# Kernel optimization log

Hardware: AMD Instinct MI355X
Metric: run time of the kernel (lower is better)

Reference implementation:

```python
import jax, jax.numpy as jnp
import numpy as np

N, E, D, H, ED, L = 50000, 800000, 256, 8, 16, 6
C = D // H  # 32
NEG_SLOPE = 0.2
EPS = 1e-5


def setup_inputs() -> dict:
    key = jax.random.key(0)
    ks = jax.random.split(key, 16)
    f32 = jnp.float32
    return {
        "x": jax.random.normal(ks[0], (N, D), f32),
        "edge_index": jax.random.randint(ks[1], (2, E), 0, N, dtype=jnp.int64),
        "edge_attr": jax.random.normal(ks[2], (E, ED), f32),
        # shared GATConv params (single conv reused every step, as in the source)
        "W": jax.random.normal(ks[3], (D, D), f32) / np.sqrt(D),
        "att_src": jax.random.normal(ks[4], (H, C), f32) * 0.05,
        "att_dst": jax.random.normal(ks[5], (H, C), f32) * 0.05,
        "att_edge": jax.random.normal(ks[6], (H, C), f32) * 0.05,
        "W_edge": jax.random.normal(ks[7], (ED, D), f32) / np.sqrt(ED),
        "bias": jnp.zeros((D,), f32),
        # per-step FFN + LayerNorm params
        "ffn_w1": jax.random.normal(ks[8], (L, D, 4 * D), f32) / np.sqrt(D),
        "ffn_b1": jnp.zeros((L, 4 * D), f32),
        "ffn_w2": jax.random.normal(ks[9], (L, 4 * D, D), f32) / np.sqrt(4 * D),
        "ffn_b2": jnp.zeros((L, D), f32),
        "ln1_g": jnp.ones((L, D), f32),
        "ln1_b": jnp.zeros((L, D), f32),
        "ln2_g": jnp.ones((L, D), f32),
        "ln2_b": jnp.zeros((L, D), f32),
    }


def _layernorm(x, g, b):
    mu = jnp.mean(x, -1, keepdims=True)
    var = jnp.mean(jnp.square(x - mu), -1, keepdims=True)
    return (x - mu) * jax.lax.rsqrt(var + EPS) * g + b


def _gat_conv(m, edge_index, edge_attr, W, att_src, att_dst, att_edge, W_edge, bias):
    n = m.shape[0]
    x_proj = (m @ W).reshape(n, H, C)  # [N,H,C]
    # add self loops; edge_attr fill_value='mean' (PyG default): mean of incoming edge feats
    src0, dst0 = edge_index[0], edge_index[1]
    deg = jax.ops.segment_sum(jnp.ones_like(dst0, jnp.float32), dst0, n)
    ea_mean = jax.ops.segment_sum(edge_attr, dst0, n) / jnp.maximum(deg, 1.0)[:, None]
    loop = jnp.arange(n, dtype=src0.dtype)
    src = jnp.concatenate([src0, loop])
    dst = jnp.concatenate([dst0, loop])
    ea = jnp.concatenate([edge_attr, ea_mean], 0)
    e_proj = (ea @ W_edge).reshape(-1, H, C)  # [E+N,H,C]
    a_src = jnp.sum(x_proj * att_src, -1)  # [N,H]
    a_dst = jnp.sum(x_proj * att_dst, -1)  # [N,H]
    a_edge = jnp.sum(e_proj * att_edge, -1)  # [E+N,H]
    alpha = jax.nn.leaky_relu(a_src[src] + a_dst[dst] + a_edge, NEG_SLOPE)
    # softmax over edges grouped by destination node
    amax = jax.ops.segment_max(alpha, dst, n)  # every node has a self loop
    ex = jnp.exp(alpha - amax[dst])
    denom = jax.ops.segment_sum(ex, dst, n)
    attn = ex / denom[dst]  # [E+N,H]
    msg = x_proj[src] * attn[:, :, None]  # [E+N,H,C]
    out = jax.ops.segment_sum(msg, dst, n).reshape(n, H * C)
    return out + bias


def reference(x, edge_index, edge_attr, W, att_src, att_dst, att_edge, W_edge, bias,
              ffn_w1, ffn_b1, ffn_w2, ffn_b2, ln1_g, ln1_b, ln2_g, ln2_b):
    m = x
    for i in range(L):
        g = _gat_conv(m, edge_index, edge_attr, W, att_src, att_dst, att_edge, W_edge, bias)
        m = _layernorm(g + m, ln1_g[i], ln1_b[i])  # dropout is identity in eval
        h = jax.nn.relu(m @ ffn_w1[i] + ffn_b1[i]) @ ffn_w2[i] + ffn_b2[i]
        m = _layernorm(h + m, ln2_g[i], ln2_b[i])
    return m
```

## Files before the change

### kernel.cpp

```cpp
#include <hip/hip_runtime.h>
#include <math.h>

#define NN 50000
#define MP 50048
#define EE 800000
#define DD 256
#define HH 8
#define CC 32
#define EDIMK 16
#define LL 6
#define HID 1024
#define NEG 0.2f
#define LNEPS 1e-5f
#define NPARTS ((NN + 255) / 256)

using short8   = __attribute__((ext_vector_type(8))) short;
using ushort8  = __attribute__((ext_vector_type(8))) unsigned short;
using floatx4  = __attribute__((ext_vector_type(4))) float;

static __device__ __forceinline__ float4 ld4(const float* p) {
    return *reinterpret_cast<const float4*>(p);
}
static __device__ __forceinline__ void st4(float* p, float4 v) {
    *reinterpret_cast<float4*>(p) = v;
}
static __device__ __forceinline__ float b2f(unsigned short u) {
    union { unsigned int i; float f; } v; v.i = ((unsigned int)u) << 16; return v.f;
}
static __device__ __forceinline__ unsigned short f2b(float f) {
    union { float f; unsigned int i; } v; v.f = f;
    unsigned int r = (v.i + 0x7fffu + ((v.i >> 16) & 1u)) >> 16;
    return (unsigned short)r;
}
static __device__ __forceinline__ void gload_lds16(const ushort* g, ushort* l) {
    __builtin_amdgcn_global_load_lds((const __attribute__((address_space(1))) void*)g,
                                     (__attribute__((address_space(3))) void*)l, 16, 0, 0);
}

__global__ void k_weh(const float* __restrict__ W_edge, const float* __restrict__ att_edge,
                      float* __restrict__ w_eh) {
    int t = threadIdx.x;
    if (t < EDIMK * HH) {
        int k = t >> 3, h = t & 7;
        float s = 0.f;
        for (int c = 0; c < CC; ++c) s += W_edge[k * DD + h * CC + c] * att_edge[h * CC + c];
        w_eh[t] = s;
    }
}

__global__ void k_edge_pre(const float* __restrict__ edge_attr, const int* __restrict__ ei,
                           const float* __restrict__ w_eh, float* __restrict__ a_edge,
                           int* __restrict__ deg) {
    __shared__ float sw[EDIMK * HH];
    if (threadIdx.x < EDIMK * HH) sw[threadIdx.x] = w_eh[threadIdx.x];
    __syncthreads();
    int e = blockIdx.x * blockDim.x + threadIdx.x;
    if (e >= EE) return;
    float ea[EDIMK];
#pragma unroll
    for (int k4 = 0; k4 < EDIMK; k4 += 4) {
        float4 v = ld4(edge_attr + (size_t)e * EDIMK + k4);
        ea[k4] = v.x; ea[k4 + 1] = v.y; ea[k4 + 2] = v.z; ea[k4 + 3] = v.w;
    }
#pragma unroll
    for (int h = 0; h < HH; ++h) {
        float s = 0.f;
#pragma unroll
        for (int k = 0; k < EDIMK; ++k) s += ea[k] * sw[k * HH + h];
        a_edge[(size_t)e * HH + h] = s;
    }
    atomicAdd(&deg[ei[EE + e]], 1);
}

__global__ __launch_bounds__(256) void k_scan1(const int* __restrict__ deg,
                                               int* __restrict__ rowptr,
                                               int* __restrict__ part) {
    __shared__ int wsum[4];
    int tid = threadIdx.x, wid = tid >> 6, lane = tid & 63;
    int g = blockIdx.x * 256 + tid;
    int v = (g < NN) ? deg[g] : 0;
    int s = v;
#pragma unroll
    for (int off = 1; off < 64; off <<= 1) {
        int t = __shfl_up(s, off, 64);
        if (lane >= off) s += t;
    }
    if (lane == 63) wsum[wid] = s;
    __syncthreads();
    int woff = 0;
    for (int i = 0; i < wid; ++i) woff += wsum[i];
    s += woff;
    if (g < NN) rowptr[g + 1] = s;
    if (tid == 255) part[blockIdx.x] = s;
}
__global__ __launch_bounds__(256) void k_scan2(int* __restrict__ part) {
    __shared__ int wsum[4];
    int tid = threadIdx.x, wid = tid >> 6, lane = tid & 63;
    int v = (tid < NPARTS) ? part[tid] : 0;
    int s = v;
#pragma unroll
    for (int off = 1; off < 64; off <<= 1) {
        int t = __shfl_up(s, off, 64);
        if (lane >= off) s += t;
    }
    if (lane == 63) wsum[wid] = s;
    __syncthreads();
    int woff = 0;
    for (int i = 0; i < wid; ++i) woff += wsum[i];
    s += woff;
    if (tid < NPARTS) part[tid] = s - v;
}
__global__ __launch_bounds__(256) void k_scan3(int* __restrict__ rowptr,
                                               const int* __restrict__ part) {
    int g = blockIdx.x * 256 + threadIdx.x;
    if (g == 0) rowptr[0] = 0;
    if (g < NN) rowptr[g + 1] += part[blockIdx.x];
}

__global__ void k_scatter(const int* __restrict__ ei, const int* __restrict__ rowptr,
                          int* __restrict__ cursor, int* __restrict__ s_src,
                          int* __restrict__ s_eid) {
    int e = blockIdx.x * blockDim.x + threadIdx.x;
    if (e >= EE) return;
    int dst = ei[EE + e];
    int p = rowptr[dst] + atomicAdd(&cursor[dst], 1);
    s_src[p] = ei[e];
    s_eid[p] = e;
}

__global__ void k_permute(const int* __restrict__ s_eid, const float* __restrict__ a_edge,
                          float* __restrict__ ae_csr) {
    size_t t = (size_t)blockIdx.x * blockDim.x + threadIdx.x;
    if (t >= (size_t)EE * HH) return;
    ae_csr[t] = a_edge[(size_t)s_eid[t >> 3] * HH + (t & 7)];
}

__global__ void k_selfmean(const int* __restrict__ rowptr, const float* __restrict__ ae_csr,
                           float* __restrict__ a_self) {
    int t = blockIdx.x * blockDim.x + threadIdx.x;
    if (t >= NN * HH) return;
    int n = t >> 3, h = t & 7;
    int k0 = rowptr[n], k1 = rowptr[n + 1];
    float s = 0.f;
    for (int k = k0; k < k1; ++k) s += ae_csr[(size_t)k * HH + h];
    int d = k1 - k0; if (d < 1) d = 1;
    a_self[t] = s / (float)d;
}

__global__ __launch_bounds__(1024) void k_trans(const float* __restrict__ src,
                                                ushort* __restrict__ dst, int K, int N) {
    __shared__ float s[32][33];
    const float* S = src + (size_t)blockIdx.z * K * N;
    ushort* D = dst + (size_t)blockIdx.z * K * N;
    int n0 = blockIdx.x * 32, k0 = blockIdx.y * 32;
    s[threadIdx.y][threadIdx.x] = S[(size_t)(k0 + threadIdx.y) * N + n0 + threadIdx.x];
    __syncthreads();
    D[(size_t)(n0 + threadIdx.y) * K + k0 + threadIdx.x] = f2b(s[threadIdx.x][threadIdx.y]);
}

__global__ void k_cvt(const float* __restrict__ x, float* __restrict__ m,
                      ushort* __restrict__ mb) {
    int t = blockIdx.x * blockDim.x + threadIdx.x;
    if (t >= NN * DD) return;
    float v = x[t];
    m[t] = v;
    mb[t] = f2b(v);
}

__global__ __launch_bounds__(256) void k_gemm_bf16(const ushort* __restrict__ A,
                                                   const ushort* __restrict__ Bt,
                                                   const float* __restrict__ bias,
                                                   void* __restrict__ Cout,
                                                   int Nc, int K, int mode) {
    __shared__ ushort As[128 * 64];
    __shared__ ushort Bs[128 * 64];
    int tid = threadIdx.x;
    int w = tid >> 6, lane = tid & 63;
    int tileM = blockIdx.y * 128, tileN = blockIdx.x * 128;
    const ushort* gA[4]; const ushort* gB[4];
    ushort* lA[4]; ushort* lB[4];
#pragma unroll
    for (int p = 0; p < 4; ++p) {
        int c = (p * 4 + w) * 64 + lane;
        int row = c >> 3, slot = c & 7;
        int gs = slot ^ (row & 7);
        gA[p] = A + (size_t)(tileM + row) * K + gs * 8;
        gB[p] = Bt + (size_t)(tileN + row) * K + gs * 8;
        lA[p] = As + (size_t)c * 8;
        lB[p] = Bs + (size_t)c * 8;
    }
    int wr = w >> 1, wc = w & 1;
    int fr = lane & 15, q = lane >> 4;
    floatx4 acc[4][4] = {};
    for (int k0 = 0; k0 < K; k0 += 64) {
        __syncthreads();
#pragma unroll
        for (int p = 0; p < 4; ++p) gload_lds16(gA[p] + k0, lA[p]);
#pragma unroll
        for (int p = 0; p < 4; ++p) gload_lds16(gB[p] + k0, lB[p]);
        __syncthreads();
#pragma unroll
        for (int kc = 0; kc < 2; ++kc) {
            int ps = ((kc * 4 + q) ^ (fr & 7)) * 8;
            short8 af[4], bf[4];
#pragma unroll
            for (int i = 0; i < 4; ++i)
                af[i] = *(const short8*)(As + (wr * 64 + i * 16 + fr) * 64 + ps);
#pragma unroll
            for (int j = 0; j < 4; ++j)
                bf[j] = *(const short8*)(Bs + (wc * 64 + j * 16 + fr) * 64 + ps);
#pragma unroll
            for (int i = 0; i < 4; ++i)
#pragma unroll
                for (int j = 0; j < 4; ++j)
                    acc[i][j] = __builtin_amdgcn_mfma_f32_16x16x32_bf16(af[i], bf[j], acc[i][j], 0, 0, 0);
        }
    }
    int rbase = tileM + wr * 64 + q * 4;
    int cbase = tileN + wc * 64 + fr;
#pragma unroll
    for (int j = 0; j < 4; ++j) {
        int col = cbase + j * 16;
        float bb = (mode != 1) ? bias[col] : 0.f;
#pragma unroll
        for (int i = 0; i < 4; ++i) {
            int row = rbase + i * 16;
#pragma unroll
            for (int r = 0; r < 4; ++r) {
                float v = acc[i][j][r] + bb;
                if (mode == 2 && v < 0.f) v = 0.f;
                ((ushort*)Cout)[(size_t)(row + r) * Nc + col] = f2b(v);
            }
        }
    }
}

__global__ __launch_bounds__(256) void k_gemm2_ln(const ushort* __restrict__ A,
                                                  const ushort* __restrict__ Bt,
                                                  const float* __restrict__ bias,
                                                  const float* __restrict__ gma,
                                                  const float* __restrict__ bta,
                                                  float* __restrict__ m,
                                                  ushort* __restrict__ mb,
                                                  int rowsValid) {
    __shared__ ushort As[64 * 64];
    __shared__ ushort Bs[256 * 64];
    __shared__ float redS[64][4];
    __shared__ float redQ[64][4];
    const int K = HID;
    int tid = threadIdx.x;
    int w = tid >> 6, lane = tid & 63;
    int tileM = blockIdx.x * 64;
    int rA = tid >> 3, sl = tid & 7;
    int gs = sl ^ (rA & 7);
    const ushort* gA = A + (size_t)(tileM + rA) * K + gs * 8;
    const ushort* gB = Bt + (size_t)rA * K + gs * 8;
    ushort* lA = As + (size_t)tid * 8;
    ushort* lB = Bs + (size_t)tid * 8;
    int fr = lane & 15, q = lane >> 4;
    floatx4 acc[4][4] = {};
    for (int k0 = 0; k0 < K; k0 += 64) {
        __syncthreads();
        gload_lds16(gA + k0, lA);
        gload_lds16(gA + (size_t)32 * K + k0, lA + 256 * 8);
#pragma unroll
        for (int p = 0; p < 8; ++p)
            gload_lds16(gB + (size_t)p * 32 * K + k0, lB + (size_t)p * 256 * 8);
        __syncthreads();
#pragma unroll
        for (int kc = 0; kc < 2; ++kc) {
            int ps = ((kc * 4 + q) ^ (fr & 7)) * 8;
            short8 af[4], bf[4];
#pragma unroll
            for (int i = 0; i < 4; ++i)
                af[i] = *(const short8*)(As + (i * 16 + fr) * 64 + ps);
#pragma unroll
            for (int j = 0; j < 4; ++j)
                bf[j] = *(const short8*)(Bs + (w * 64 + j * 16 + fr) * 64 + ps);
#pragma unroll
            for (int i = 0; i < 4; ++i)
#pragma unroll
                for (int j = 0; j < 4; ++j)
                    acc[i][j] = __builtin_amdgcn_mfma_f32_16x16x32_bf16(af[i], bf[j], acc[i][j], 0, 0, 0);
        }
    }
    int colb = w * 64 + fr;
    float bw[4], gw[4], btw[4];
#pragma unroll
    for (int j = 0; j < 4; ++j) {
        bw[j] = bias[colb + j * 16];
        gw[j] = gma[colb + j * 16];
        btw[j] = bta[colb + j * 16];
    }
#pragma unroll
    for (int i = 0; i < 4; ++i) {
#pragma unroll
        for (int rr = 0; rr < 4; ++rr) {
            int lrow = i * 16 + q * 4 + rr;
            int grow = tileM + lrow;
            bool valid = grow < rowsValid;
            float s = 0.f, s2 = 0.f;
#pragma unroll
            for (int j = 0; j < 4; ++j) {
                float rres = valid ? m[(size_t)grow * DD + colb + j * 16] : 0.f;
                float gv = acc[i][j][rr] + bw[j] + rres;
                acc[i][j][rr] = gv;
                s += gv; s2 += gv * gv;
            }
#pragma unroll
            for (int msk = 1; msk < 16; msk <<= 1) {
                s += __shfl_xor(s, msk, 16);
                s2 += __shfl_xor(s2, msk, 16);
            }
            if (fr == 0) { redS[lrow][w] = s; redQ[lrow][w] = s2; }
        }
    }
    __syncthreads();
#pragma unroll
    for (int i = 0; i < 4; ++i) {
#pragma unroll
        for (int rr = 0; rr < 4; ++rr) {
            int lrow = i * 16 + q * 4 + rr;
            int grow = tileM + lrow;
            if (grow >= rowsValid) continue;
            float su = redS[lrow][0] + redS[lrow][1] + redS[lrow][2] + redS[lrow][3];
            float sq = redQ[lrow][0] + redQ[lrow][1] + redQ[lrow][2] + redQ[lrow][3];
            float mu = su * (1.0f / DD);
            float var = sq * (1.0f / DD) - mu * mu;
            float rs = rsqrtf(var + LNEPS);
#pragma unroll
            for (int j = 0; j < 4; ++j) {
                float v = (acc[i][j][rr] - mu) * rs * gw[j] + btw[j];
                size_t idx = (size_t)grow * DD + colb + j * 16;
                m[idx] = v;
                mb[idx] = f2b(v);
            }
        }
    }
}

__global__ void k_srcdst(const ushort* __restrict__ xb, const float* __restrict__ att_src,
                         const float* __restrict__ att_dst, float* __restrict__ a_src,
                         float* __restrict__ a_dst) {
    __shared__ float ss[DD], sd[DD];
    int tid = threadIdx.x;
    if (tid < DD) { ss[tid] = att_src[tid]; sd[tid] = att_dst[tid]; }
    __syncthreads();
    int t = blockIdx.x * blockDim.x + tid;
    if (t >= NN * HH) return;
    int n = t >> 3, h = t & 7;
    const ushort* xp = xb + (size_t)n * DD + h * CC;
    float s1 = 0.f, s2 = 0.f;
#pragma unroll
    for (int c = 0; c < CC; c += 4) {
        ushort4 u = *(const ushort4*)(xp + c);
        float vx = b2f(u.x), vy = b2f(u.y), vz = b2f(u.z), vw = b2f(u.w);
        int b = h * CC + c;
        s1 += vx * ss[b] + vy * ss[b + 1] + vz * ss[b + 2] + vw * ss[b + 3];
        s2 += vx * sd[b] + vy * sd[b + 1] + vz * sd[b + 2] + vw * sd[b + 3];
    }
    a_src[t] = s1;
    a_dst[t] = s2;
}

__global__ __launch_bounds__(256) void k_agg(const ushort* __restrict__ xb,
                                             const float* __restrict__ a_src,
                                             const float* __restrict__ a_dst,
                                             const float* __restrict__ a_self,
                                             const int* __restrict__ rowptr,
                                             const int* __restrict__ s_src,
                                             const float* __restrict__ ae_csr,
                                             const float* __restrict__ bias,
                                             const float* __restrict__ gma,
                                             const float* __restrict__ bta,
                                             float* __restrict__ m,
                                             ushort* __restrict__ mb) {
    int wid = (blockIdx.x * blockDim.x + threadIdx.x) >> 6;
    int lane = threadIdx.x & 63;
    int n = wid * 2 + (lane >> 5);
    if (n >= NN) return;
    int hl = lane & 31, h = hl >> 2, c8 = hl * 8;
    float adn = a_dst[n * HH + h];
    float al0 = a_src[n * HH + h] + adn + a_self[n * HH + h];
    al0 = al0 > 0.f ? al0 : NEG * al0;
    float w0 = __expf(al0);
    ushort8 xs = *(const ushort8*)(xb + (size_t)n * DD + c8);
    float acc[8];
#pragma unroll
    for (int i = 0; i < 8; ++i) acc[i] = w0 * b2f(xs[i]);
    float den = w0;
    int k = rowptr[n], k1 = rowptr[n + 1];
    for (; k + 3 < k1; k += 4) {
        int s0 = s_src[k], s1 = s_src[k + 1], s2 = s_src[k + 2], s3 = s_src[k + 3];
        float e0 = ae_csr[(size_t)k * HH + h];
        float e1 = ae_csr[(size_t)(k + 1) * HH + h];
        float e2 = ae_csr[(size_t)(k + 2) * HH + h];
        float e3 = ae_csr[(size_t)(k + 3) * HH + h];
        float t0 = a_src[(size_t)s0 * HH + h] + adn + e0;
        float t1 = a_src[(size_t)s1 * HH + h] + adn + e1;
        float t2 = a_src[(size_t)s2 * HH + h] + adn + e2;
        float t3 = a_src[(size_t)s3 * HH + h] + adn + e3;
        ushort8 v0 = *(const ushort8*)(xb + (size_t)s0 * DD + c8);
        ushort8 v1 = *(const ushort8*)(xb + (size_t)s1 * DD + c8);
        ushort8 v2 = *(const ushort8*)(xb + (size_t)s2 * DD + c8);
        ushort8 v3 = *(const ushort8*)(xb + (size_t)s3 * DD + c8);
        t0 = t0 > 0.f ? t0 : NEG * t0;
        t1 = t1 > 0.f ? t1 : NEG * t1;
        t2 = t2 > 0.f ? t2 : NEG * t2;
        t3 = t3 > 0.f ? t3 : NEG * t3;
        float wv0 = __expf(t0), wv1 = __expf(t1), wv2 = __expf(t2), wv3 = __expf(t3);
        den += (wv0 + wv1) + (wv2 + wv3);
#pragma unroll
        for (int i = 0; i < 8; ++i)
            acc[i] += (wv0 * b2f(v0[i]) + wv1 * b2f(v1[i])) + (wv2 * b2f(v2[i]) + wv3 * b2f(v3[i]));
    }
    for (; k < k1; ++k) {
        int s0 = s_src[k];
        float t0 = a_src[(size_t)s0 * HH + h] + adn + ae_csr[(size_t)k * HH + h];
        t0 = t0 > 0.f ? t0 : NEG * t0;
        float wv0 = __expf(t0);
        ushort8 v0 = *(const ushort8*)(xb + (size_t)s0 * DD + c8);
        den += wv0;
#pragma unroll
        for (int i = 0; i < 8; ++i) acc[i] += wv0 * b2f(v0[i]);
    }
    float inv = 1.f / den;
    size_t base = (size_t)n * DD + c8;
    float4 mr0 = ld4(m + base), mr1 = ld4(m + base + 4);
    float4 b0 = ld4(bias + c8), b1 = ld4(bias + c8 + 4);
    float g[8];
    g[0] = acc[0] * inv + b0.x + mr0.x; g[1] = acc[1] * inv + b0.y + mr0.y;
    g[2] = acc[2] * inv + b0.z + mr0.z; g[3] = acc[3] * inv + b0.w + mr0.w;
    g[4] = acc[4] * inv + b1.x + mr1.x; g[5] = acc[5] * inv + b1.y + mr1.y;
    g[6] = acc[6] * inv + b1.z + mr1.z; g[7] = acc[7] * inv + b1.w + mr1.w;
    float s = 0.f;
#pragma unroll
    for (int i = 0; i < 8; ++i) s += g[i];
#pragma unroll
    for (int off = 16; off; off >>= 1) s += __shfl_xor(s, off, 64);
    float mu = s * (1.0f / DD);
    float qv = 0.f;
#pragma unroll
    for (int i = 0; i < 8; ++i) { g[i] -= mu; qv += g[i] * g[i]; }
#pragma unroll
    for (int off = 16; off; off >>= 1) qv += __shfl_xor(qv, off, 64);
    float rs = rsqrtf(qv * (1.0f / DD) + LNEPS);
    float4 g0 = ld4(gma + c8), g1 = ld4(gma + c8 + 4);
    float4 bb0 = ld4(bta + c8), bb1 = ld4(bta + c8 + 4);
    float o[8];
    o[0] = g[0] * rs * g0.x + bb0.x; o[1] = g[1] * rs * g0.y + bb0.y;
    o[2] = g[2] * rs * g0.z + bb0.z; o[3] = g[3] * rs * g0.w + bb0.w;
    o[4] = g[4] * rs * g1.x + bb1.x; o[5] = g[5] * rs * g1.y + bb1.y;
    o[6] = g[6] * rs * g1.z + bb1.z; o[7] = g[7] * rs * g1.w + bb1.w;
    st4(m + base, make_float4(o[0], o[1], o[2], o[3]));
    st4(m + base + 4, make_float4(o[4], o[5], o[6], o[7]));
    ushort8 ob;
#pragma unroll
    for (int i = 0; i < 8; ++i) ob[i] = f2b(o[i]);
    *reinterpret_cast<ushort8*>(mb + base) = ob;
}

extern "C" void kernel_launch(void* const* d_in, const int* in_sizes, int n_in,
                              void* d_out, int out_size, void* d_ws, size_t ws_size,
                              hipStream_t stream) {
    const float* x        = (const float*)d_in[0];
    const int*   ei       = (const int*)d_in[1];
    const float* edge_attr= (const float*)d_in[2];
    const float* W        = (const float*)d_in[3];
    const float* att_src  = (const float*)d_in[4];
    const float* att_dst  = (const float*)d_in[5];
    const float* att_edge = (const float*)d_in[6];
    const float* W_edge   = (const float*)d_in[7];
    const float* bias     = (const float*)d_in[8];
    const float* ffn_w1   = (const float*)d_in[9];
    const float* ffn_b1   = (const float*)d_in[10];
    const float* ffn_w2   = (const float*)d_in[11];
    const float* ffn_b2   = (const float*)d_in[12];
    const float* ln1_g    = (const float*)d_in[13];
    const float* ln1_b    = (const float*)d_in[14];
    const float* ln2_g    = (const float*)d_in[15];
    const float* ln2_b    = (const float*)d_in[16];
    float* m = (float*)d_out;

    char* wp = (char*)d_ws;
    auto alloc = [&](size_t bytes) -> char* {
        char* p = wp;
        wp += (bytes + 255) & ~(size_t)255;
        return p;
    };
    float*  a_edge = (float*)alloc((size_t)EE * HH * 4);
    float*  ae_csr = (float*)alloc((size_t)EE * HH * 4);
    float*  a_self = (float*)alloc((size_t)NN * HH * 4);
    float*  a_src  = (float*)alloc((size_t)NN * HH * 4);
    float*  a_dst  = (float*)alloc((size_t)NN * HH * 4);
    int*    deg    = (int*)alloc((size_t)NN * 4);
    int*    rowptr = (int*)alloc((size_t)(NN + 1) * 4);
    int*    cursor = (int*)alloc((size_t)NN * 4);
    int*    part   = (int*)alloc((size_t)NPARTS * 4);
    int*    s_src  = (int*)alloc((size_t)EE * 4);
    int*    s_eid  = (int*)alloc((size_t)EE * 4);
    float*  w_eh   = (float*)alloc((size_t)EDIMK * HH * 4);
    ushort* Wt     = (ushort*)alloc((size_t)DD * DD * 2);
    ushort* w1t    = (ushort*)alloc((size_t)LL * DD * HID * 2);
    ushort* w2t    = (ushort*)alloc((size_t)LL * HID * DD * 2);
    ushort* xprojb = (ushort*)alloc((size_t)MP * DD * 2);
    ushort* m_b    = (ushort*)alloc((size_t)MP * DD * 2);
    size_t used = (size_t)(wp - (char*)d_ws);
    size_t avail = ws_size > used ? ws_size - used : 0;
    size_t maxrows = avail / ((size_t)HID * 2);
    int chunkP = (int)((maxrows / 128) * 128);
    if (chunkP < 128) chunkP = 128;
    if (chunkP > MP) chunkP = MP;
    ushort* h1b = (ushort*)wp;

    hipMemsetAsync(deg, 0, (size_t)NN * 4, stream);
    hipMemsetAsync(cursor, 0, (size_t)NN * 4, stream);

    k_weh<<<1, 128, 0, stream>>>(W_edge, att_edge, w_eh);
    k_edge_pre<<<(EE + 255) / 256, 256, 0, stream>>>(edge_attr, ei, w_eh, a_edge, deg);
    k_scan1<<<NPARTS, 256, 0, stream>>>(deg, rowptr, part);
    k_scan2<<<1, 256, 0, stream>>>(part);
    k_scan3<<<NPARTS, 256, 0, stream>>>(rowptr, part);
    k_scatter<<<(EE + 255) / 256, 256, 0, stream>>>(ei, rowptr, cursor, s_src, s_eid);
    k_permute<<<(EE * HH + 255) / 256, 256, 0, stream>>>(s_eid, a_edge, ae_csr);
    k_selfmean<<<(NN * HH + 255) / 256, 256, 0, stream>>>(rowptr, ae_csr, a_self);
    k_trans<<<dim3(DD / 32, DD / 32, 1), dim3(32, 32), 0, stream>>>(W, Wt, DD, DD);
    k_trans<<<dim3(HID / 32, DD / 32, LL), dim3(32, 32), 0, stream>>>(ffn_w1, w1t, DD, HID);
    k_trans<<<dim3(DD / 32, HID / 32, LL), dim3(32, 32), 0, stream>>>(ffn_w2, w2t, HID, DD);
    k_cvt<<<(NN * DD + 255) / 256, 256, 0, stream>>>(x, m, m_b);

    for (int i = 0; i < LL; ++i) {
        k_gemm_bf16<<<dim3(DD / 128, MP / 128), 256, 0, stream>>>(m_b, Wt, nullptr, xprojb, DD, DD, 1);
        k_srcdst<<<(NN * HH + 255) / 256, 256, 0, stream>>>(xprojb, att_src, att_dst, a_src, a_dst);
        k_agg<<<((NN + 1) / 2 * 64 + 255) / 256, 256, 0, stream>>>(xprojb, a_src, a_dst, a_self,
                                                                   rowptr, s_src, ae_csr, bias,
                                                                   ln1_g + i * DD, ln1_b + i * DD, m, m_b);
        for (int r0 = 0; r0 < MP; r0 += chunkP) {
            int rows = (MP - r0) < chunkP ? (MP - r0) : chunkP;
            k_gemm_bf16<<<dim3(HID / 128, rows / 128), 256, 0, stream>>>(
                m_b + (size_t)r0 * DD, w1t + (size_t)i * DD * HID,
                ffn_b1 + (size_t)i * HID, h1b, HID, DD, 2);
            k_gemm2_ln<<<rows / 64, 256, 0, stream>>>(
                h1b, w2t + (size_t)i * HID * DD, ffn_b2 + (size_t)i * DD,
                ln2_g + i * DD, ln2_b + i * DD,
                m + (size_t)r0 * DD, m_b + (size_t)r0 * DD, NN - r0);
        }
    }
}
```

Baseline: 1.857 ms.

## Fuse FFN up/down GEMMs into one kernel and write edge logits directly to CSR order

Replaces the two-GEMM FFN (up-projection writing a bf16 hidden buffer, then down-projection with fused LayerNorm) with one kernel. Each 64-row tile keeps its activations in LDS, computes the hidden layer in 32-column chunks with bias and ReLU, and accumulates the down-projection on the fly, so the large hidden tensor never goes through global memory. The edge preprocessing now records each edge's CSR position and writes attention logits straight into CSR order, removing the a_edge buffer and the permute kernel. The trade-off is a fused kernel with small 32-wide chunks, three barriers per chunk and no prefetch of weight tiles, which may underuse the matrix units.

```diff
diff --git a/kernel.cpp b/kernel.cpp
--- a/kernel.cpp
+++ b/kernel.cpp
@@ -48,27 +48,9 @@
     }
 }
 
-__global__ void k_edge_pre(const float* __restrict__ edge_attr, const int* __restrict__ ei,
-                           const float* __restrict__ w_eh, float* __restrict__ a_edge,
-                           int* __restrict__ deg) {
-    __shared__ float sw[EDIMK * HH];
-    if (threadIdx.x < EDIMK * HH) sw[threadIdx.x] = w_eh[threadIdx.x];
-    __syncthreads();
+__global__ void k_deg(const int* __restrict__ ei, int* __restrict__ deg) {
     int e = blockIdx.x * blockDim.x + threadIdx.x;
     if (e >= EE) return;
-    float ea[EDIMK];
-#pragma unroll
-    for (int k4 = 0; k4 < EDIMK; k4 += 4) {
-        float4 v = ld4(edge_attr + (size_t)e * EDIMK + k4);
-        ea[k4] = v.x; ea[k4 + 1] = v.y; ea[k4 + 2] = v.z; ea[k4 + 3] = v.w;
-    }
-#pragma unroll
-    for (int h = 0; h < HH; ++h) {
-        float s = 0.f;
-#pragma unroll
-        for (int k = 0; k < EDIMK; ++k) s += ea[k] * sw[k * HH + h];
-        a_edge[(size_t)e * HH + h] = s;
-    }
     atomicAdd(&deg[ei[EE + e]], 1);
 }
 
@@ -119,20 +101,37 @@
 
 __global__ void k_scatter(const int* __restrict__ ei, const int* __restrict__ rowptr,
                           int* __restrict__ cursor, int* __restrict__ s_src,
-                          int* __restrict__ s_eid) {
+                          int* __restrict__ perm) {
     int e = blockIdx.x * blockDim.x + threadIdx.x;
     if (e >= EE) return;
     int dst = ei[EE + e];
     int p = rowptr[dst] + atomicAdd(&cursor[dst], 1);
     s_src[p] = ei[e];
-    s_eid[p] = e;
-}
-
-__global__ void k_permute(const int* __restrict__ s_eid, const float* __restrict__ a_edge,
-                          float* __restrict__ ae_csr) {
-    size_t t = (size_t)blockIdx.x * blockDim.x + threadIdx.x;
-    if (t >= (size_t)EE * HH) return;
-    ae_csr[t] = a_edge[(size_t)s_eid[t >> 3] * HH + (t & 7)];
+    perm[e] = p;
+}
+
+__global__ void k_edge_csr(const float* __restrict__ edge_attr, const int* __restrict__ perm,
+                           const float* __restrict__ w_eh, float* __restrict__ ae_csr) {
+    __shared__ float sw[EDIMK * HH];
+    if (threadIdx.x < EDIMK * HH) sw[threadIdx.x] = w_eh[threadIdx.x];
+    __syncthreads();
+    int e = blockIdx.x * blockDim.x + threadIdx.x;
+    if (e >= EE) return;
+    float ea[EDIMK];
+#pragma unroll
+    for (int k4 = 0; k4 < EDIMK; k4 += 4) {
+        float4 v = ld4(edge_attr + (size_t)e * EDIMK + k4);
+        ea[k4] = v.x; ea[k4 + 1] = v.y; ea[k4 + 2] = v.z; ea[k4 + 3] = v.w;
+    }
+    int p = perm[e];
+    float* out = ae_csr + (size_t)p * HH;
+#pragma unroll
+    for (int h = 0; h < HH; ++h) {
+        float s = 0.f;
+#pragma unroll
+        for (int k = 0; k < EDIMK; ++k) s += ea[k] * sw[k * HH + h];
+        out[h] = s;
+    }
 }
 
 __global__ void k_selfmean(const int* __restrict__ rowptr, const float* __restrict__ ae_csr,
@@ -228,67 +227,101 @@
 #pragma unroll
             for (int r = 0; r < 4; ++r) {
                 float v = acc[i][j][r] + bb;
-                if (mode == 2 && v < 0.f) v = 0.f;
                 ((ushort*)Cout)[(size_t)(row + r) * Nc + col] = f2b(v);
             }
         }
     }
 }
 
-__global__ __launch_bounds__(256) void k_gemm2_ln(const ushort* __restrict__ A,
-                                                  const ushort* __restrict__ Bt,
-                                                  const float* __restrict__ bias,
-                                                  const float* __restrict__ gma,
-                                                  const float* __restrict__ bta,
-                                                  float* __restrict__ m,
-                                                  ushort* __restrict__ mb,
-                                                  int rowsValid) {
-    __shared__ ushort As[64 * 64];
-    __shared__ ushort Bs[256 * 64];
+__global__ __launch_bounds__(256) void k_mlp(const ushort* __restrict__ A,
+                                             const ushort* __restrict__ w1,
+                                             const ushort* __restrict__ w2,
+                                             const float* __restrict__ b1,
+                                             const float* __restrict__ b2,
+                                             const float* __restrict__ gma,
+                                             const float* __restrict__ bta,
+                                             float* __restrict__ m,
+                                             ushort* __restrict__ mb) {
+    __shared__ ushort As[64 * 256];
+    __shared__ ushort W1s[32 * 256];
+    __shared__ ushort W2s[256 * 32];
+    __shared__ ushort Hs[64 * 32];
     __shared__ float redS[64][4];
     __shared__ float redQ[64][4];
-    const int K = HID;
     int tid = threadIdx.x;
     int w = tid >> 6, lane = tid & 63;
+    int fr = lane & 15, q = lane >> 4;
     int tileM = blockIdx.x * 64;
-    int rA = tid >> 3, sl = tid & 7;
-    int gs = sl ^ (rA & 7);
-    const ushort* gA = A + (size_t)(tileM + rA) * K + gs * 8;
-    const ushort* gB = Bt + (size_t)rA * K + gs * 8;
-    ushort* lA = As + (size_t)tid * 8;
-    ushort* lB = Bs + (size_t)tid * 8;
-    int fr = lane & 15, q = lane >> 4;
-    floatx4 acc[4][4] = {};
-    for (int k0 = 0; k0 < K; k0 += 64) {
+#pragma unroll
+    for (int p = 0; p < 8; ++p) {
+        int c = p * 256 + tid;
+        int row = c >> 5, sl = c & 31;
+        int l = sl ^ (row & 7);
+        gload_lds16(A + (size_t)(tileM + row) * DD + l * 8, As + (size_t)c * 8);
+    }
+    floatx4 acc2[4][4] = {};
+    for (int ch = 0; ch < 32; ++ch) {
+#pragma unroll
+        for (int p = 0; p < 4; ++p) {
+            int c = p * 256 + tid;
+            int row = c >> 5, sl = c & 31;
+            int l = sl ^ (row & 7);
+            gload_lds16(w1 + (size_t)(ch * 32 + row) * DD + l * 8, W1s + (size_t)c * 8);
+        }
+#pragma unroll
+        for (int p = 0; p < 4; ++p) {
+            int c = p * 256 + tid;
+            int row = c >> 2, sl = c & 3;
+            int l = sl ^ (row & 3);
+            gload_lds16(w2 + (size_t)row * HID + ch * 32 + l * 8, W2s + (size_t)c * 8);
+        }
         __syncthreads();
-        gload_lds16(gA + k0, lA);
-        gload_lds16(gA + (size_t)32 * K + k0, lA + 256 * 8);
-#pragma unroll
-        for (int p = 0; p < 8; ++p)
-            gload_lds16(gB + (size_t)p * 32 * K + k0, lB + (size_t)p * 256 * 8);
+        floatx4 acc1[2] = {};
+#pragma unroll
+        for (int ks = 0; ks < 8; ++ks) {
+            int ps = ((ks * 4 + q) ^ (fr & 7)) * 8;
+            short8 af = *(const short8*)(As + (w * 16 + fr) * 256 + ps);
+#pragma unroll
+            for (int j = 0; j < 2; ++j) {
+                short8 bf = *(const short8*)(W1s + (j * 16 + fr) * 256 + ps);
+                acc1[j] = __builtin_amdgcn_mfma_f32_16x16x32_bf16(af, bf, acc1[j], 0, 0, 0);
+            }
+        }
+#pragma unroll
+        for (int j = 0; j < 2; ++j) {
+            float bb = b1[ch * 32 + j * 16 + fr];
+            int l = j * 2 + (fr >> 3);
+#pragma unroll
+            for (int r = 0; r < 4; ++r) {
+                float v = acc1[j][r] + bb;
+                v = v > 0.f ? v : 0.f;
+                int row = w * 16 + q * 4 + r;
+                Hs[row * 32 + ((l ^ r) * 8) + (fr & 7)] = f2b(v);
+            }
+        }
         __syncthreads();
-#pragma unroll
-        for (int kc = 0; kc < 2; ++kc) {
-            int ps = ((kc * 4 + q) ^ (fr & 7)) * 8;
-            short8 af[4], bf[4];
+        {
+            int ps2 = (q ^ (fr & 3)) * 8;
+            short8 af2[4], bf2[4];
 #pragma unroll
             for (int i = 0; i < 4; ++i)
-                af[i] = *(const short8*)(As + (i * 16 + fr) * 64 + ps);
+                af2[i] = *(const short8*)(Hs + (i * 16 + fr) * 32 + ps2);
 #pragma unroll
             for (int j = 0; j < 4; ++j)
-                bf[j] = *(const short8*)(Bs + (w * 64 + j * 16 + fr) * 64 + ps);
+                bf2[j] = *(const short8*)(W2s + (w * 64 + j * 16 + fr) * 32 + ps2);
 #pragma unroll
             for (int i = 0; i < 4; ++i)
 #pragma unroll
                 for (int j = 0; j < 4; ++j)
-                    acc[i][j] = __builtin_amdgcn_mfma_f32_16x16x32_bf16(af[i], bf[j], acc[i][j], 0, 0, 0);
-        }
+                    acc2[i][j] = __builtin_amdgcn_mfma_f32_16x16x32_bf16(af2[i], bf2[j], acc2[i][j], 0, 0, 0);
+        }
+        __syncthreads();
     }
     int colb = w * 64 + fr;
     float bw[4], gw[4], btw[4];
 #pragma unroll
     for (int j = 0; j < 4; ++j) {
-        bw[j] = bias[colb + j * 16];
+        bw[j] = b2[colb + j * 16];
         gw[j] = gma[colb + j * 16];
         btw[j] = bta[colb + j * 16];
     }
@@ -298,13 +331,13 @@
         for (int rr = 0; rr < 4; ++rr) {
             int lrow = i * 16 + q * 4 + rr;
             int grow = tileM + lrow;
-            bool valid = grow < rowsValid;
+            bool valid = grow < NN;
             float s = 0.f, s2 = 0.f;
 #pragma unroll
             for (int j = 0; j < 4; ++j) {
                 float rres = valid ? m[(size_t)grow * DD + colb + j * 16] : 0.f;
-                float gv = acc[i][j][rr] + bw[j] + rres;
-                acc[i][j][rr] = gv;
+                float gv = acc2[i][j][rr] + bw[j] + rres;
+                acc2[i][j][rr] = gv;
                 s += gv; s2 += gv * gv;
             }
 #pragma unroll
@@ -322,7 +355,7 @@
         for (int rr = 0; rr < 4; ++rr) {
             int lrow = i * 16 + q * 4 + rr;
             int grow = tileM + lrow;
-            if (grow >= rowsValid) continue;
+            if (grow >= NN) continue;
             float su = redS[lrow][0] + redS[lrow][1] + redS[lrow][2] + redS[lrow][3];
             float sq = redQ[lrow][0] + redQ[lrow][1] + redQ[lrow][2] + redQ[lrow][3];
             float mu = su * (1.0f / DD);
@@ -330,7 +363,7 @@
             float rs = rsqrtf(var + LNEPS);
 #pragma unroll
             for (int j = 0; j < 4; ++j) {
-                float v = (acc[i][j][rr] - mu) * rs * gw[j] + btw[j];
+                float v = (acc2[i][j][rr] - mu) * rs * gw[j] + btw[j];
                 size_t idx = (size_t)grow * DD + colb + j * 16;
                 m[idx] = v;
                 mb[idx] = f2b(v);
@@ -488,7 +521,6 @@
         wp += (bytes + 255) & ~(size_t)255;
         return p;
     };
-    float*  a_edge = (float*)alloc((size_t)EE * HH * 4);
     float*  ae_csr = (float*)alloc((size_t)EE * HH * 4);
     float*  a_self = (float*)alloc((size_t)NN * HH * 4);
     float*  a_src  = (float*)alloc((size_t)NN * HH * 4);
@@ -498,31 +530,24 @@
     int*    cursor = (int*)alloc((size_t)NN * 4);
     int*    part   = (int*)alloc((size_t)NPARTS * 4);
     int*    s_src  = (int*)alloc((size_t)EE * 4);
-    int*    s_eid  = (int*)alloc((size_t)EE * 4);
+    int*    perm   = (int*)alloc((size_t)EE * 4);
     float*  w_eh   = (float*)alloc((size_t)EDIMK * HH * 4);
     ushort* Wt     = (ushort*)alloc((size_t)DD * DD * 2);
     ushort* w1t    = (ushort*)alloc((size_t)LL * DD * HID * 2);
     ushort* w2t    = (ushort*)alloc((size_t)LL * HID * DD * 2);
     ushort* xprojb = (ushort*)alloc((size_t)MP * DD * 2);
     ushort* m_b    = (ushort*)alloc((size_t)MP * DD * 2);
-    size_t used = (size_t)(wp - (char*)d_ws);
-    size_t avail = ws_size > used ? ws_size - used : 0;
-    size_t maxrows = avail / ((size_t)HID * 2);
-    int chunkP = (int)((maxrows / 128) * 128);
-    if (chunkP < 128) chunkP = 128;
-    if (chunkP > MP) chunkP = MP;
-    ushort* h1b = (ushort*)wp;
 
     hipMemsetAsync(deg, 0, (size_t)NN * 4, stream);
     hipMemsetAsync(cursor, 0, (size_t)NN * 4, stream);
 
     k_weh<<<1, 128, 0, stream>>>(W_edge, att_edge, w_eh);
-    k_edge_pre<<<(EE + 255) / 256, 256, 0, stream>>>(edge_attr, ei, w_eh, a_edge, deg);
+    k_deg<<<(EE + 255) / 256, 256, 0, stream>>>(ei, deg);
     k_scan1<<<NPARTS, 256, 0, stream>>>(deg, rowptr, part);
     k_scan2<<<1, 256, 0, stream>>>(part);
     k_scan3<<<NPARTS, 256, 0, stream>>>(rowptr, part);
-    k_scatter<<<(EE + 255) / 256, 256, 0, stream>>>(ei, rowptr, cursor, s_src, s_eid);
-    k_permute<<<(EE * HH + 255) / 256, 256, 0, stream>>>(s_eid, a_edge, ae_csr);
+    k_scatter<<<(EE + 255) / 256, 256, 0, stream>>>(ei, rowptr, cursor, s_src, perm);
+    k_edge_csr<<<(EE + 255) / 256, 256, 0, stream>>>(edge_attr, perm, w_eh, ae_csr);
     k_selfmean<<<(NN * HH + 255) / 256, 256, 0, stream>>>(rowptr, ae_csr, a_self);
     k_trans<<<dim3(DD / 32, DD / 32, 1), dim3(32, 32), 0, stream>>>(W, Wt, DD, DD);
     k_trans<<<dim3(HID / 32, DD / 32, LL), dim3(32, 32), 0, stream>>>(ffn_w1, w1t, DD, HID);
@@ -535,15 +560,9 @@
         k_agg<<<((NN + 1) / 2 * 64 + 255) / 256, 256, 0, stream>>>(xprojb, a_src, a_dst, a_self,
                                                                    rowptr, s_src, ae_csr, bias,
                                                                    ln1_g + i * DD, ln1_b + i * DD, m, m_b);
-        for (int r0 = 0; r0 < MP; r0 += chunkP) {
-            int rows = (MP - r0) < chunkP ? (MP - r0) : chunkP;
-            k_gemm_bf16<<<dim3(HID / 128, rows / 128), 256, 0, stream>>>(
-                m_b + (size_t)r0 * DD, w1t + (size_t)i * DD * HID,
-                ffn_b1 + (size_t)i * HID, h1b, HID, DD, 2);
-            k_gemm2_ln<<<rows / 64, 256, 0, stream>>>(
-                h1b, w2t + (size_t)i * HID * DD, ffn_b2 + (size_t)i * DD,
-                ln2_g + i * DD, ln2_b + i * DD,
-                m + (size_t)r0 * DD, m_b + (size_t)r0 * DD, NN - r0);
-        }
-    }
-}
+        k_mlp<<<MP / 64, 256, 0, stream>>>(m_b, w1t + (size_t)i * DD * HID,
+                                           w2t + (size_t)i * HID * DD,
+                                           ffn_b1 + (size_t)i * HID, ffn_b2 + (size_t)i * DD,
+                                           ln2_g + i * DD, ln2_b + i * DD, m, m_b);
+    }
+}
```

Result: slower. 1.921 ms (+3.4%).
